# Performance work log

Hardware: AMD Instinct MI355X
Metric: run time of the kernel (lower is better)

## Reference

```python
import jax, jax.numpy as jnp
import numpy as np

IN_DIM = 128
HID = 64  # hidden_dim
N_NODES = 100000
N_EDGES = 1000000

def setup_inputs() -> dict:
    key = jax.random.key(0)
    ks = jax.random.split(key, 8)
    z = jax.random.normal(ks[0], (N_NODES, IN_DIM), dtype=jnp.float32)
    edge_index = jax.random.randint(ks[1], (2, N_EDGES), 0, N_NODES, dtype=jnp.int64)
    # MLP params: Linear(2*in_dim, hid) -> ReLU -> Linear(hid, hid//2) -> ReLU -> Linear(hid//2, 1)
    def lin(k, fan_in, fan_out):
        bound = 1.0 / np.sqrt(fan_in)
        kw, kb = jax.random.split(k)
        W = jax.random.uniform(kw, (fan_in, fan_out), minval=-bound, maxval=bound, dtype=jnp.float32)
        b = jax.random.uniform(kb, (fan_out,), minval=-bound, maxval=bound, dtype=jnp.float32)
        return W, b
    W1, b1 = lin(ks[2], 2 * IN_DIM, HID)
    W2, b2 = lin(ks[3], HID, HID // 2)
    W3, b3 = lin(ks[4], HID // 2, 1)
    return {"z": z, "edge_index": edge_index, "W1": W1, "b1": b1, "W2": W2, "b2": b2, "W3": W3, "b3": b3}

def reference(z, edge_index, W1, b1, W2, b2, W3, b3):
    # gather endpoint embeddings: [E, in_dim] each
    zi = z[edge_index[0]]
    zj = z[edge_index[1]]
    h = jnp.concatenate([zi, zj], axis=-1)          # [E, 2*in_dim]
    h = jax.nn.relu(h @ W1 + b1)                     # [E, hid] (dropout = identity in eval)
    h = jax.nn.relu(h @ W2 + b2)                     # [E, hid//2]
    logits = (h @ W3 + b3).squeeze(-1)               # [E]
    return jax.nn.sigmoid(logits)
```

## Files before the change

### kernel.cpp

```cpp
#include <hip/hip_runtime.h>
#include <hip/hip_bf16.h>

typedef __attribute__((ext_vector_type(8))) short short8;
typedef __attribute__((ext_vector_type(4))) float f32x4;

__device__ __forceinline__ unsigned short f32_bf16(float f) {
  unsigned u = __float_as_uint(f);
  u += 0x7fffu + ((u >> 16) & 1u);
  return (unsigned short)(u >> 16);
}

__device__ __forceinline__ short8 cvt8(float4 v0, float4 v1) {
  short8 f;
  f[0] = (short)f32_bf16(v0.x); f[1] = (short)f32_bf16(v0.y);
  f[2] = (short)f32_bf16(v0.z); f[3] = (short)f32_bf16(v0.w);
  f[4] = (short)f32_bf16(v1.x); f[5] = (short)f32_bf16(v1.y);
  f[6] = (short)f32_bf16(v1.z); f[7] = (short)f32_bf16(v1.w);
  return f;
}

__device__ __forceinline__ unsigned addrelu2(unsigned uw, unsigned vw, float blo, float bhi) {
  float ulo = __uint_as_float(uw << 16);
  float uhi = __uint_as_float(uw & 0xffff0000u);
  float vlo = __uint_as_float(vw << 16);
  float vhi = __uint_as_float(vw & 0xffff0000u);
  float slo = ulo + vlo + blo; slo = slo > 0.f ? slo : 0.f;
  float shi = uhi + vhi + bhi; shi = shi > 0.f ? shi : 0.f;
  return ((unsigned)f32_bf16(shi) << 16) | (unsigned)f32_bf16(slo);
}

template <int CTRL>
__device__ __forceinline__ float dpp_add(float x) {
  int y = __builtin_amdgcn_update_dpp(0, __float_as_int(x), CTRL, 0xf, 0xf, true);
  return x + __int_as_float(y);
}
__device__ __forceinline__ float row_sum16(float x) {
  x = dpp_add<0x118>(x);
  x = dpp_add<0x114>(x);
  x = dpp_add<0x112>(x);
  x = dpp_add<0x111>(x);
  return x;
}

__global__ __launch_bounds__(256, 2) void uv_kernel(
    const float* __restrict__ z, const float* __restrict__ W1,
    unsigned short* __restrict__ uv, int nNodes) {
  __shared__ unsigned short w1l[32 * 64 * 8];
  const int tid = threadIdx.x;
  const int wv  = tid >> 6;
  const int l   = tid & 63;
  const int l15 = l & 15;
  const int q   = l >> 4;

#pragma unroll
  for (int pp = 0; pp < 8; ++pp) {
    int p = wv * 8 + pp;
    int c = p >> 3, t = p & 7;
    short8 f;
#pragma unroll
    for (int j = 0; j < 8; ++j) {
      int k = c * 32 + q * 8 + j;
      int n = l15 * 8 + t;
      int row = (n < 64) ? k : (k + 128);
      f[j] = (short)f32_bf16(W1[row * 64 + (n & 63)]);
    }
    *(short8*)(w1l + (p * 64 + l) * 8) = f;
  }
  __syncthreads();

  const int nTiles = (nNodes + 15) >> 4;
  const int stride = gridDim.x * 4;
  for (int tile = blockIdx.x * 4 + wv; tile < nTiles; tile += stride) {
    int node = tile * 16 + l15;
    node = node < nNodes ? node : nNodes - 1;
    const float* zr = z + (size_t)node * 128;
    short8 a[4];
#pragma unroll
    for (int c = 0; c < 4; ++c) {
      int off = c * 32 + q * 8;
      a[c] = cvt8(*(const float4*)(zr + off), *(const float4*)(zr + off + 4));
    }
    f32x4 acc[8];
#pragma unroll
    for (int t = 0; t < 8; ++t) { acc[t][0] = 0.f; acc[t][1] = 0.f; acc[t][2] = 0.f; acc[t][3] = 0.f; }
#pragma unroll
    for (int c = 0; c < 4; ++c)
#pragma unroll
      for (int t = 0; t < 8; ++t) {
        short8 wf = *(const short8*)(w1l + ((c * 8 + t) * 64 + l) * 8);
        acc[t] = __builtin_amdgcn_mfma_f32_16x16x32_bf16(a[c], wf, acc[t], 0, 0, 0);
      }
#pragma unroll
    for (int r = 0; r < 4; ++r) {
      int no = tile * 16 + q * 4 + r;
      if (no < nNodes) {
        union { unsigned short us[8]; uint4 u4; } pk;
#pragma unroll
        for (int t = 0; t < 8; ++t) pk.us[t] = f32_bf16(acc[t][r]);
        *(uint4*)(uv + (size_t)no * 128 + l15 * 8) = pk.u4;
      }
    }
  }
}

__global__ __launch_bounds__(256, 2) void lp_edge(
    const unsigned short* __restrict__ uv, const int* __restrict__ ei,
    const float* __restrict__ b1,
    const float* __restrict__ W2, const float* __restrict__ b2,
    const float* __restrict__ W3, const float* __restrict__ b3,
    float* __restrict__ out, int nEdges) {
  const int tid = threadIdx.x;
  const int wv  = tid >> 6;
  const int l   = tid & 63;
  const int l15 = l & 15;
  const int q   = l >> 4;

  short8 w2f[2][2];
#pragma unroll
  for (int c = 0; c < 2; ++c)
#pragma unroll
    for (int t = 0; t < 2; ++t) {
      short8 f;
#pragma unroll
      for (int j = 0; j < 8; ++j)
        f[j] = (short)f32_bf16(W2[(c * 32 + q * 8 + j) * 32 + (t * 16 + l15)]);
      w2f[c][t] = f;
    }
  float bb2[2];
#pragma unroll
  for (int t = 0; t < 2; ++t) bb2[t] = b2[t * 16 + l15];
  const float w3a = W3[l15], w3b = W3[16 + l15], b3v = b3[0];
  float b1f0[8], b1f1[8];
#pragma unroll
  for (int j = 0; j < 8; ++j) { b1f0[j] = b1[q * 8 + j]; b1f1[j] = b1[32 + q * 8 + j]; }

  const int nIter = (nEdges + 15) >> 4;
  const int stride = gridDim.x * 4;
  int iter = blockIdx.x * 4 + wv;

  int cS = 0, cD = 0;
  if (iter < nIter) {
    int e = iter * 16 + l15;
    e = e < nEdges ? e : nEdges - 1;
    cS = ei[e];
    cD = ei[nEdges + e];
  }

  for (; iter < nIter; iter += stride) {
    const unsigned short* us = uv + (size_t)cS * 128;
    const unsigned short* vd = uv + (size_t)cD * 128 + 64;
    uint4 au0 = *(const uint4*)(us + q * 8);
    uint4 au1 = *(const uint4*)(us + 32 + q * 8);
    uint4 av0 = *(const uint4*)(vd + q * 8);
    uint4 av1 = *(const uint4*)(vd + 32 + q * 8);

    int nit = iter + stride;
    int nS = cS, nD = cD;
    if (nit < nIter) {
      int e = nit * 16 + l15;
      e = e < nEdges ? e : nEdges - 1;
      nS = ei[e];
      nD = ei[nEdges + e];
    }

    union { unsigned u[4]; short8 s; } f0, f1;
    f0.u[0] = addrelu2(au0.x, av0.x, b1f0[0], b1f0[1]);
    f0.u[1] = addrelu2(au0.y, av0.y, b1f0[2], b1f0[3]);
    f0.u[2] = addrelu2(au0.z, av0.z, b1f0[4], b1f0[5]);
    f0.u[3] = addrelu2(au0.w, av0.w, b1f0[6], b1f0[7]);
    f1.u[0] = addrelu2(au1.x, av1.x, b1f1[0], b1f1[1]);
    f1.u[1] = addrelu2(au1.y, av1.y, b1f1[2], b1f1[3]);
    f1.u[2] = addrelu2(au1.z, av1.z, b1f1[4], b1f1[5]);
    f1.u[3] = addrelu2(au1.w, av1.w, b1f1[6], b1f1[7]);

    f32x4 acc2[2];
#pragma unroll
    for (int t = 0; t < 2; ++t) {
      acc2[t][0] = bb2[t]; acc2[t][1] = bb2[t]; acc2[t][2] = bb2[t]; acc2[t][3] = bb2[t];
    }
#pragma unroll
    for (int t = 0; t < 2; ++t) {
      acc2[t] = __builtin_amdgcn_mfma_f32_16x16x32_bf16(f0.s, w2f[0][t], acc2[t], 0, 0, 0);
      acc2[t] = __builtin_amdgcn_mfma_f32_16x16x32_bf16(f1.s, w2f[1][t], acc2[t], 0, 0, 0);
    }

    float p[4];
#pragma unroll
    for (int r = 0; r < 4; ++r) {
      float h0 = acc2[0][r]; h0 = h0 > 0.f ? h0 : 0.f;
      float h1v = acc2[1][r]; h1v = h1v > 0.f ? h1v : 0.f;
      p[r] = row_sum16(h0 * w3a + h1v * w3b);
    }

    if (l15 == 15) {
      int eb = iter * 16 + q * 4;
      float4 o;
      o.x = 1.f / (1.f + __expf(-(p[0] + b3v)));
      o.y = 1.f / (1.f + __expf(-(p[1] + b3v)));
      o.z = 1.f / (1.f + __expf(-(p[2] + b3v)));
      o.w = 1.f / (1.f + __expf(-(p[3] + b3v)));
      if (eb + 3 < nEdges) {
        *(float4*)(out + eb) = o;
      } else {
        if (eb < nEdges)     out[eb]     = o.x;
        if (eb + 1 < nEdges) out[eb + 1] = o.y;
        if (eb + 2 < nEdges) out[eb + 2] = o.z;
      }
    }

    cS = nS; cD = nD;
  }
}

__global__ void lp_naive(const float* __restrict__ z, const int* __restrict__ ei,
                         const float* __restrict__ W1, const float* __restrict__ b1,
                         const float* __restrict__ W2, const float* __restrict__ b2,
                         const float* __restrict__ W3, const float* __restrict__ b3,
                         float* __restrict__ out, int nEdges) {
  int e = blockIdx.x * 256 + threadIdx.x;
  if (e >= nEdges) return;
  int s = ei[e], d = ei[nEdges + e];
  float h1[64], h2[32];
  for (int k = 0; k < 64; ++k) {
    float a = b1[k];
    for (int i = 0; i < 128; ++i) a += z[(size_t)s * 128 + i] * W1[i * 64 + k];
    for (int i = 0; i < 128; ++i) a += z[(size_t)d * 128 + i] * W1[(128 + i) * 64 + k];
    h1[k] = a > 0.f ? a : 0.f;
  }
  for (int k = 0; k < 32; ++k) {
    float a = b2[k];
    for (int i = 0; i < 64; ++i) a += h1[i] * W2[i * 32 + k];
    h2[k] = a > 0.f ? a : 0.f;
  }
  float lg = b3[0];
  for (int i = 0; i < 32; ++i) lg += h2[i] * W3[i];
  out[e] = 1.f / (1.f + __expf(-lg));
}

extern "C" void kernel_launch(void* const* d_in, const int* in_sizes, int n_in,
                              void* d_out, int out_size, void* d_ws, size_t ws_size,
                              hipStream_t stream) {
  const float* z  = (const float*)d_in[0];
  const int* ei   = (const int*)d_in[1];
  const float* W1 = (const float*)d_in[2];
  const float* b1 = (const float*)d_in[3];
  const float* W2 = (const float*)d_in[4];
  const float* b2 = (const float*)d_in[5];
  const float* W3 = (const float*)d_in[6];
  const float* b3 = (const float*)d_in[7];
  float* out = (float*)d_out;

  const int nZ = in_sizes[0];
  const int nNodes = nZ / 128;
  const int nEdges = in_sizes[1] / 2;

  if (ws_size >= (size_t)nNodes * 128 * sizeof(unsigned short)) {
    unsigned short* uvp = (unsigned short*)d_ws;
    uv_kernel<<<1024, 256, 0, stream>>>(z, W1, uvp, nNodes);
    lp_edge<<<1024, 256, 0, stream>>>(uvp, ei, b1, W2, b2, W3, b3, out, nEdges);
  } else {
    lp_naive<<<(nEdges + 255) / 256, 256, 0, stream>>>(z, ei, W1, b1, W2, b2, W3, b3, out, nEdges);
  }
}
```

Before: 146.2 us.

## Deepen gather prefetch pipeline, use packed bf16 converts, raise edge-kernel occupancy

The edge kernel now prefetches the next iteration's gathered uv rows, plus the edge indices two iterations ahead, so gather latency overlaps with compute. It also uses nontemporal loads for indices and nontemporal stores for outputs. Software float-to-bf16 rounding is replaced with the packed v_cvt_pk_bf16_f32 instruction. Launch bounds are raised to 4 blocks per CU with a 2048-block grid, and the uv grid is sized to the tile count. The deeper pipeline holds more live registers, which may conflict with the higher occupancy target and cause spills.

Result: no change. 146.6 us (+0.2%).

```diff
diff --git a/kernel.cpp b/kernel.cpp
--- a/kernel.cpp
+++ b/kernel.cpp
@@ -10,13 +10,19 @@
   return (unsigned short)(u >> 16);
 }
 
+__device__ __forceinline__ unsigned cvt_pk_bf16(float lo, float hi) {
+  unsigned r;
+  asm("v_cvt_pk_bf16_f32 %0, %1, %2" : "=v"(r) : "v"(lo), "v"(hi));
+  return r;
+}
+
 __device__ __forceinline__ short8 cvt8(float4 v0, float4 v1) {
-  short8 f;
-  f[0] = (short)f32_bf16(v0.x); f[1] = (short)f32_bf16(v0.y);
-  f[2] = (short)f32_bf16(v0.z); f[3] = (short)f32_bf16(v0.w);
-  f[4] = (short)f32_bf16(v1.x); f[5] = (short)f32_bf16(v1.y);
-  f[6] = (short)f32_bf16(v1.z); f[7] = (short)f32_bf16(v1.w);
-  return f;
+  union { unsigned u[4]; short8 s; } f;
+  f.u[0] = cvt_pk_bf16(v0.x, v0.y);
+  f.u[1] = cvt_pk_bf16(v0.z, v0.w);
+  f.u[2] = cvt_pk_bf16(v1.x, v1.y);
+  f.u[3] = cvt_pk_bf16(v1.z, v1.w);
+  return f.s;
 }
 
 __device__ __forceinline__ unsigned addrelu2(unsigned uw, unsigned vw, float blo, float bhi) {
@@ -26,7 +32,7 @@
   float vhi = __uint_as_float(vw & 0xffff0000u);
   float slo = ulo + vlo + blo; slo = slo > 0.f ? slo : 0.f;
   float shi = uhi + vhi + bhi; shi = shi > 0.f ? shi : 0.f;
-  return ((unsigned)f32_bf16(shi) << 16) | (unsigned)f32_bf16(slo);
+  return cvt_pk_bf16(slo, shi);
 }
 
 template <int CTRL>
@@ -94,16 +100,16 @@
     for (int r = 0; r < 4; ++r) {
       int no = tile * 16 + q * 4 + r;
       if (no < nNodes) {
-        union { unsigned short us[8]; uint4 u4; } pk;
-#pragma unroll
-        for (int t = 0; t < 8; ++t) pk.us[t] = f32_bf16(acc[t][r]);
+        union { unsigned u[4]; uint4 u4; } pk;
+#pragma unroll
+        for (int t = 0; t < 4; ++t) pk.u[t] = cvt_pk_bf16(acc[2 * t][r], acc[2 * t + 1][r]);
         *(uint4*)(uv + (size_t)no * 128 + l15 * 8) = pk.u4;
       }
     }
   }
 }
 
-__global__ __launch_bounds__(256, 2) void lp_edge(
+__global__ __launch_bounds__(256, 4) void lp_edge(
     const unsigned short* __restrict__ uv, const int* __restrict__ ei,
     const float* __restrict__ b1,
     const float* __restrict__ W2, const float* __restrict__ b2,
@@ -136,32 +142,34 @@
 
   const int nIter = (nEdges + 15) >> 4;
   const int stride = gridDim.x * 4;
-  int iter = blockIdx.x * 4 + wv;
-
-  int cS = 0, cD = 0;
-  if (iter < nIter) {
-    int e = iter * 16 + l15;
-    e = e < nEdges ? e : nEdges - 1;
-    cS = ei[e];
-    cD = ei[nEdges + e];
-  }
-
-  for (; iter < nIter; iter += stride) {
+  const int it0 = blockIdx.x * 4 + wv;
+
+  int e0 = it0 * 16 + l15; e0 = e0 < nEdges ? e0 : nEdges - 1;
+  int cS = __builtin_nontemporal_load(ei + e0);
+  int cD = __builtin_nontemporal_load(ei + nEdges + e0);
+  uint4 au0, au1, av0, av1;
+  {
     const unsigned short* us = uv + (size_t)cS * 128;
     const unsigned short* vd = uv + (size_t)cD * 128 + 64;
-    uint4 au0 = *(const uint4*)(us + q * 8);
-    uint4 au1 = *(const uint4*)(us + 32 + q * 8);
-    uint4 av0 = *(const uint4*)(vd + q * 8);
-    uint4 av1 = *(const uint4*)(vd + 32 + q * 8);
-
-    int nit = iter + stride;
-    int nS = cS, nD = cD;
-    if (nit < nIter) {
-      int e = nit * 16 + l15;
-      e = e < nEdges ? e : nEdges - 1;
-      nS = ei[e];
-      nD = ei[nEdges + e];
-    }
+    au0 = *(const uint4*)(us + q * 8);
+    au1 = *(const uint4*)(us + 32 + q * 8);
+    av0 = *(const uint4*)(vd + q * 8);
+    av1 = *(const uint4*)(vd + 32 + q * 8);
+  }
+  int e1 = (it0 + stride) * 16 + l15; e1 = e1 < nEdges ? e1 : nEdges - 1;
+  int nS = __builtin_nontemporal_load(ei + e1);
+  int nD = __builtin_nontemporal_load(ei + nEdges + e1);
+
+  for (int iter = it0; iter < nIter; iter += stride) {
+    const unsigned short* usn = uv + (size_t)nS * 128;
+    const unsigned short* vdn = uv + (size_t)nD * 128 + 64;
+    uint4 bu0 = *(const uint4*)(usn + q * 8);
+    uint4 bu1 = *(const uint4*)(usn + 32 + q * 8);
+    uint4 bv0 = *(const uint4*)(vdn + q * 8);
+    uint4 bv1 = *(const uint4*)(vdn + 32 + q * 8);
+    int e2 = (iter + 2 * stride) * 16 + l15; e2 = e2 < nEdges ? e2 : nEdges - 1;
+    int mS = __builtin_nontemporal_load(ei + e2);
+    int mD = __builtin_nontemporal_load(ei + nEdges + e2);
 
     union { unsigned u[4]; short8 s; } f0, f1;
     f0.u[0] = addrelu2(au0.x, av0.x, b1f0[0], b1f0[1]);
@@ -194,21 +202,22 @@
 
     if (l15 == 15) {
       int eb = iter * 16 + q * 4;
-      float4 o;
-      o.x = 1.f / (1.f + __expf(-(p[0] + b3v)));
-      o.y = 1.f / (1.f + __expf(-(p[1] + b3v)));
-      o.z = 1.f / (1.f + __expf(-(p[2] + b3v)));
-      o.w = 1.f / (1.f + __expf(-(p[3] + b3v)));
+      f32x4 o;
+      o[0] = 1.f / (1.f + __expf(-(p[0] + b3v)));
+      o[1] = 1.f / (1.f + __expf(-(p[1] + b3v)));
+      o[2] = 1.f / (1.f + __expf(-(p[2] + b3v)));
+      o[3] = 1.f / (1.f + __expf(-(p[3] + b3v)));
       if (eb + 3 < nEdges) {
-        *(float4*)(out + eb) = o;
+        __builtin_nontemporal_store(o, (f32x4*)(out + eb));
       } else {
-        if (eb < nEdges)     out[eb]     = o.x;
-        if (eb + 1 < nEdges) out[eb + 1] = o.y;
-        if (eb + 2 < nEdges) out[eb + 2] = o.z;
+        if (eb < nEdges)     out[eb]     = o[0];
+        if (eb + 1 < nEdges) out[eb + 1] = o[1];
+        if (eb + 2 < nEdges) out[eb + 2] = o[2];
       }
     }
 
-    cS = nS; cD = nD;
+    au0 = bu0; au1 = bu1; av0 = bv0; av1 = bv1;
+    nS = mS; nD = mD;
   }
 }
 
@@ -256,8 +265,11 @@
 
   if (ws_size >= (size_t)nNodes * 128 * sizeof(unsigned short)) {
     unsigned short* uvp = (unsigned short*)d_ws;
-    uv_kernel<<<1024, 256, 0, stream>>>(z, W1, uvp, nNodes);
-    lp_edge<<<1024, 256, 0, stream>>>(uvp, ei, b1, W2, b2, W3, b3, out, nEdges);
+    int nTiles = (nNodes + 15) >> 4;
+    int uvGrid = (nTiles + 7) >> 3;
+    if (uvGrid > 1024) uvGrid = 1024;
+    uv_kernel<<<uvGrid, 256, 0, stream>>>(z, W1, uvp, nNodes);
+    lp_edge<<<2048, 256, 0, stream>>>(uvp, ei, b1, W2, b2, W3, b3, out, nEdges);
   } else {
     lp_naive<<<(nEdges + 255) / 256, 256, 0, stream>>>(z, ei, W1, b1, W2, b2, W3, b3, out, nEdges);
   }
```
